# Performance work log

Measured on AMD Instinct MI355X. Metric: run time of the kernel, lower is better.

## Reference

```python
import jax, jax.numpy as jnp
import numpy as np

B, S, D, H, KD, VD, HID, L, V, OUTN = 16, 512, 512, 8, 64, 64, 2048, 4, 32000, 128
EPS = 1e-5


def _layer_norm(x, g, b):
    m = jnp.mean(x, axis=-1, keepdims=True)
    v = jnp.mean(jnp.square(x - m), axis=-1, keepdims=True)
    return (x - m) * jax.lax.rsqrt(v + EPS) * g + b


def _pos_encoding(seq_len, d_model):
    pos = jnp.arange(seq_len, dtype=jnp.float32)[:, None]
    div = jnp.exp(jnp.arange(0, d_model, 2, dtype=jnp.float32) * (-np.log(10000.0) / d_model))
    pe = jnp.zeros((seq_len, d_model), dtype=jnp.float32)
    pe = pe.at[:, 0::2].set(jnp.sin(pos * div))
    pe = pe.at[:, 1::2].set(jnp.cos(pos * div))
    return pe


def setup_inputs() -> dict:
    key = jax.random.key(0)
    ks = jax.random.split(key, 32)
    s = 0.02
    n = jax.random.normal
    inp = {
        "enc_inputs": jax.random.randint(ks[0], (B, S), 0, V, dtype=jnp.int32),
        "emb": n(ks[1], (V, D), jnp.float32) * s,
        # stacked per-layer params, leading dim = L
        "Wq": n(ks[2], (L, D, H * KD), jnp.float32) * s,
        "bq": jnp.zeros((L, H * KD), jnp.float32),
        "Wk": n(ks[3], (L, D, H * KD), jnp.float32) * s,
        "bk": jnp.zeros((L, H * KD), jnp.float32),
        "Wv": n(ks[4], (L, D, H * VD), jnp.float32) * s,
        "bv": jnp.zeros((L, H * VD), jnp.float32),
        "Wo": n(ks[5], (L, H * VD, D), jnp.float32) * s,
        "bo": jnp.zeros((L, D), jnp.float32),
        "ln1_g": jnp.ones((L, D), jnp.float32),
        "ln1_b": jnp.zeros((L, D), jnp.float32),
        "W1": n(ks[6], (L, D, HID), jnp.float32) * s,   # conv1d k=1 == linear
        "b1": jnp.zeros((L, HID), jnp.float32),
        "W2": n(ks[7], (L, HID, D), jnp.float32) * s,
        "b2": jnp.zeros((L, D), jnp.float32),
        "ln2_g": jnp.ones((L, D), jnp.float32),
        "ln2_b": jnp.zeros((L, D), jnp.float32),
        # flatten head created inside torch forward: [S*D, 128]
        "Wf": n(ks[8], (S * D, OUTN), jnp.float32) * s,
        "bf": jnp.zeros((OUTN,), jnp.float32),
        "Wout": n(ks[9], (OUTN, 1), jnp.float32) * s,
        "bout": jnp.zeros((1,), jnp.float32),
    }
    return inp


def _encoder(enc_inputs, emb, Wq, bq, Wk, bk, Wv, bv, Wo, bo, ln1_g, ln1_b,
             W1, b1, W2, b2, ln2_g, ln2_b, Wf, bf, Wout, bout):
    x = emb[enc_inputs] + _pos_encoding(S, D)[None, :, :]          # [B,S,D]
    pad = (enc_inputs == 0)[:, None, None, :]                      # [B,1,1,S]
    scale = 1.0 / np.sqrt(D)                                       # note: sqrt(embed_dim), as in source
    for l in range(L):
        # multi-head attention
        q = (x @ Wq[l] + bq[l]).reshape(B, S, H, KD)
        k = (x @ Wk[l] + bk[l]).reshape(B, S, H, KD)
        v = (x @ Wv[l] + bv[l]).reshape(B, S, H, VD)
        scores = jnp.einsum('bqhd,bkhd->bhqk', q, k) * scale
        scores = jnp.where(pad, -1e9, scores)
        attn = jax.nn.softmax(scores, axis=-1)
        ctx = jnp.einsum('bhqk,bkhd->bqhd', attn, v).reshape(B, S, H * VD)
        x = _layer_norm(ctx @ Wo[l] + bo[l] + x, ln1_g[l], ln1_b[l])
        # position-wise FFN (conv1d kernel_size=1)
        h = jax.nn.relu(x @ W1[l] + b1[l])
        x = _layer_norm(h @ W2[l] + b2[l] + x, ln2_g[l], ln2_b[l])
    flat = x.reshape(B, S * D)
    features = flat @ Wf + bf                                      # [B,128]
    y_score = jax.nn.sigmoid(features @ Wout + bout)               # [B,1]
    y_pred = jnp.round(y_score)
    return y_score, y_pred, features


def reference(enc_inputs, emb, Wq, bq, Wk, bk, Wv, bv, Wo, bo, ln1_g, ln1_b,
              W1, b1, W2, b2, ln2_g, ln2_b, Wf, bf, Wout, bout):
    return _encoder(enc_inputs, emb, Wq, bq, Wk, bk, Wv, bv, Wo, bo, ln1_g, ln1_b,
                    W1, b1, W2, b2, ln2_g, ln2_b, Wf, bf, Wout, bout)
```

## Files before the change

kernel.cpp:

```cpp
#include <hip/hip_runtime.h>
#include <hip/hip_bf16.h>
#include <math.h>

typedef unsigned short ushort_t;
typedef __attribute__((ext_vector_type(8))) short bf16x8;
typedef __attribute__((ext_vector_type(4))) float f32x4;

#define SCALE_QK 0.04419417382415922f
#define PE_C 0.017988946039015986f

__device__ __forceinline__ void g2lds16(const void* g, void* l) {
    __builtin_amdgcn_global_load_lds(
        (const __attribute__((address_space(1))) unsigned int*)g,
        (__attribute__((address_space(3))) unsigned int*)l,
        16, 0, 0);
}
__device__ __forceinline__ ushort_t f2bs(float v) {
    __hip_bfloat16 h = __float2bfloat16(v);
    return *reinterpret_cast<ushort_t*>(&h);
}
__device__ __forceinline__ float bs2f(ushort_t v) {
    return __uint_as_float(((unsigned int)v) << 16);
}

template<bool RELU, bool VT>
__global__ __launch_bounds__(512, 2) void gemm8(
    const ushort_t* __restrict__ A, const ushort_t* __restrict__ B,
    const float* __restrict__ bias, ushort_t* __restrict__ C,
    ushort_t* __restrict__ vt, int K, int lda, int ldb, int ldc)
{
    __shared__ ushort_t As[2][256 * 64];
    __shared__ ushort_t Bs[2][256 * 64];

    const int t = threadIdx.x;
    const int lane = t & 63, w = t >> 6;
    const int l16 = lane & 15, quad = lane >> 4;
    const int r8 = lane >> 3;
    const int kg = ((lane & 7) ^ r8) << 3;
    const int wm = (w >> 2) * 128;
    const int wn = (w & 3) * 64;
    const int m0 = blockIdx.y * 256, n0 = blockIdx.x * 256;
    const int NT = K >> 6;

    f32x4 acc[8][4];
    #pragma unroll
    for (int i = 0; i < 8; i++)
        #pragma unroll
        for (int j = 0; j < 4; j++)
            acc[i][j] = (f32x4){0.f, 0.f, 0.f, 0.f};

    auto STAGE8 = [&](int kt, int bb) {
        int k0 = kt << 6;
        #pragma unroll
        for (int ii = 0; ii < 4; ii++) {
            int rbase = w * 32 + ii * 8;
            g2lds16(A + (size_t)(m0 + rbase + r8) * lda + k0 + kg,
                    &As[bb][rbase * 64]);
            g2lds16(B + (size_t)(n0 + rbase + r8) * ldb + k0 + kg,
                    &Bs[bb][rbase * 64]);
        }
    };

    STAGE8(0, 0);
    STAGE8(1, 1);

    for (int kt = 0; kt < NT; kt++) {
        const int bb = kt & 1;
        if (kt < NT - 1)
            asm volatile("s_waitcnt vmcnt(8)" ::: "memory");
        else
            asm volatile("s_waitcnt vmcnt(0)" ::: "memory");
        __builtin_amdgcn_s_barrier();
        asm volatile("" ::: "memory");

        #pragma unroll
        for (int tt = 0; tt < 2; tt++) {
            bf16x8 af[8], bf[4];
            #pragma unroll
            for (int i = 0; i < 8; i++) {
                int row = wm + i * 16 + l16;
                af[i] = *(const bf16x8*)&As[bb][row * 64 + ((((tt << 2) + quad) ^ (row & 7)) << 3)];
            }
            #pragma unroll
            for (int j = 0; j < 4; j++) {
                int row = wn + j * 16 + l16;
                bf[j] = *(const bf16x8*)&Bs[bb][row * 64 + ((((tt << 2) + quad) ^ (row & 7)) << 3)];
            }
            #pragma unroll
            for (int i = 0; i < 8; i++)
                #pragma unroll
                for (int j = 0; j < 4; j++)
                    acc[i][j] = __builtin_amdgcn_mfma_f32_16x16x32_bf16(
                        af[i], bf[j], acc[i][j], 0, 0, 0);
        }

        asm volatile("" ::: "memory");
        __builtin_amdgcn_s_barrier();
        asm volatile("" ::: "memory");
        if (kt + 2 < NT)
            STAGE8(kt + 2, bb);
    }

    if (VT && n0 >= 1024) {
        #pragma unroll
        for (int i = 0; i < 8; i++) {
            int mbase = m0 + wm + i * 16 + quad * 4;
            int b = mbase >> 9, s = mbase & 511;
            #pragma unroll
            for (int j = 0; j < 4; j++) {
                int n = n0 + wn + j * 16 + l16;
                int hv = n - 1024;
                int h = hv >> 6, vd = hv & 63;
                float bv = bias[n];
                ushort4 pk;
                pk.x = f2bs(acc[i][j][0] + bv);
                pk.y = f2bs(acc[i][j][1] + bv);
                pk.z = f2bs(acc[i][j][2] + bv);
                pk.w = f2bs(acc[i][j][3] + bv);
                *(ushort4*)&vt[((size_t)((b << 3) + h)) * 32768 + (size_t)vd * 512 + s] = pk;
            }
        }
        return;
    }

    #pragma unroll
    for (int i = 0; i < 8; i++)
        #pragma unroll
        for (int j = 0; j < 4; j++) {
            int n = n0 + wn + j * 16 + l16;
            float bv = bias[n];
            #pragma unroll
            for (int r = 0; r < 4; r++) {
                int m = m0 + wm + i * 16 + quad * 4 + r;
                float v = acc[i][j][r] + bv;
                if (RELU) v = fmaxf(v, 0.f);
                C[(size_t)m * ldc + n] = f2bs(v);
            }
        }
}

__global__ __launch_bounds__(512) void gemmLN(
    const ushort_t* __restrict__ A, const ushort_t* __restrict__ B,
    const float* __restrict__ bias, const ushort_t* __restrict__ res,
    const float* __restrict__ g, const float* __restrict__ bt,
    ushort_t* __restrict__ X, int K, int lda)
{
    __shared__ ushort_t As[2][32 * 64];
    __shared__ ushort_t Bs[2][512 * 64];
    __shared__ float2 pst[8][32];
    __shared__ float2 rmv[32];

    const int t = threadIdx.x;
    const int lane = t & 63, w = t >> 6;
    const int l16 = lane & 15, quad = lane >> 4;
    const int r8 = lane >> 3;
    const int kg = ((lane & 7) ^ r8) << 3;
    const int wn = w * 64;
    const int m0 = blockIdx.x * 32;
    const int NT = K >> 6;

    f32x4 acc[2][4];
    #pragma unroll
    for (int i = 0; i < 2; i++)
        #pragma unroll
        for (int j = 0; j < 4; j++)
            acc[i][j] = (f32x4){0.f, 0.f, 0.f, 0.f};

    auto STAGE = [&](int kt, int bb) {
        int k0 = kt << 6;
        if (w < 4)
            g2lds16(A + (size_t)(m0 + w * 8 + r8) * lda + k0 + kg,
                    &As[bb][(w * 8) * 64]);
        #pragma unroll
        for (int ii = 0; ii < 8; ii++) {
            int rbase = w * 64 + ii * 8;
            g2lds16(B + (size_t)(rbase + r8) * K + k0 + kg,
                    &Bs[bb][rbase * 64]);
        }
    };

    STAGE(0, 0);
    STAGE(1, 1);

    for (int kt = 0; kt < NT; kt++) {
        const int bb = kt & 1;
        if (kt < NT - 1) {
            if (w < 4) asm volatile("s_waitcnt vmcnt(9)" ::: "memory");
            else       asm volatile("s_waitcnt vmcnt(8)" ::: "memory");
        } else {
            asm volatile("s_waitcnt vmcnt(0)" ::: "memory");
        }
        __builtin_amdgcn_s_barrier();
        asm volatile("" ::: "memory");

        #pragma unroll
        for (int tt = 0; tt < 2; tt++) {
            bf16x8 af[2], bf4[4];
            #pragma unroll
            for (int i = 0; i < 2; i++) {
                int row = i * 16 + l16;
                af[i] = *(const bf16x8*)&As[bb][row * 64 + ((((tt << 2) + quad) ^ (row & 7)) << 3)];
            }
            #pragma unroll
            for (int j = 0; j < 4; j++) {
                int row = wn + j * 16 + l16;
                bf4[j] = *(const bf16x8*)&Bs[bb][row * 64 + ((((tt << 2) + quad) ^ (row & 7)) << 3)];
            }
            #pragma unroll
            for (int i = 0; i < 2; i++)
                #pragma unroll
                for (int j = 0; j < 4; j++)
                    acc[i][j] = __builtin_amdgcn_mfma_f32_16x16x32_bf16(
                        af[i], bf4[j], acc[i][j], 0, 0, 0);
        }

        asm volatile("" ::: "memory");
        __builtin_amdgcn_s_barrier();
        asm volatile("" ::: "memory");
        if (kt + 2 < NT)
            STAGE(kt + 2, bb);
    }

    float rs[2][4], rq[2][4];
    #pragma unroll
    for (int i = 0; i < 2; i++)
        #pragma unroll
        for (int r = 0; r < 4; r++) { rs[i][r] = 0.f; rq[i][r] = 0.f; }

    #pragma unroll
    for (int i = 0; i < 2; i++)
        #pragma unroll
        for (int j = 0; j < 4; j++) {
            int n = wn + j * 16 + l16;
            float bvn = bias[n];
            #pragma unroll
            for (int r = 0; r < 4; r++) {
                int row = i * 16 + quad * 4 + r;
                float v = acc[i][j][r] + bvn
                        + bs2f(res[(size_t)(m0 + row) * 512 + n]);
                acc[i][j][r] = v;
                rs[i][r] += v;
                rq[i][r] += v * v;
            }
        }

    #pragma unroll
    for (int i = 0; i < 2; i++)
        #pragma unroll
        for (int r = 0; r < 4; r++) {
            #pragma unroll
            for (int off = 1; off < 16; off <<= 1) {
                rs[i][r] += __shfl_xor(rs[i][r], off);
                rq[i][r] += __shfl_xor(rq[i][r], off);
            }
            if (l16 == 0)
                pst[w][i * 16 + quad * 4 + r] = make_float2(rs[i][r], rq[i][r]);
        }
    __syncthreads();
    if (t < 32) {
        float s = 0.f, q = 0.f;
        #pragma unroll
        for (int wv = 0; wv < 8; wv++) {
            float2 p = pst[wv][t];
            s += p.x; q += p.y;
        }
        float mean = s * (1.f / 512.f);
        float var = q * (1.f / 512.f) - mean * mean;
        rmv[t] = make_float2(mean, rsqrtf(var + 1e-5f));
    }
    __syncthreads();

    #pragma unroll
    for (int i = 0; i < 2; i++)
        #pragma unroll
        for (int j = 0; j < 4; j++) {
            int n = wn + j * 16 + l16;
            float gn = g[n], btn = bt[n];
            #pragma unroll
            for (int r = 0; r < 4; r++) {
                int row = i * 16 + quad * 4 + r;
                float2 mr = rmv[row];
                float o = (acc[i][j][r] - mr.x) * mr.y * gn + btn;
                X[(size_t)(m0 + row) * 512 + n] = f2bs(o);
            }
        }
}

__global__ __launch_bounds__(256) void flash_attn(
    ushort_t* __restrict__ QKV, const ushort_t* __restrict__ Vt,
    const int* __restrict__ tok)
{
    __shared__ ushort_t Qs[128 * 64];
    __shared__ ushort_t Ks[128 * 64];
    __shared__ ushort_t Vts[64 * 128];
    __shared__ ushort_t Ps[128 * 128];

    const int bh = blockIdx.y;
    const int b = bh >> 3, h = bh & 7;
    const int q0 = blockIdx.x * 128;
    const int t = threadIdx.x;
    const int lane = t & 63, w = t >> 6;
    const int l16 = lane & 15, quad = lane >> 4;
    const int wm = w * 32;
    const size_t rowbase = (size_t)b * 512;

    {
        int r8 = lane >> 3;
        int kg = (lane & 7) ^ r8;
        #pragma unroll
        for (int ii = 0; ii < 4; ii++) {
            int rb = w * 32 + ii * 8;
            g2lds16(QKV + (rowbase + q0 + rb + r8) * 1536 + h * 64 + kg * 8,
                    &Qs[rb * 64]);
        }
    }

    f32x4 accO[2][4];
    #pragma unroll
    for (int i = 0; i < 2; i++)
        #pragma unroll
        for (int jv = 0; jv < 4; jv++)
            accO[i][jv] = (f32x4){0.f, 0.f, 0.f, 0.f};
    float lrow[2][4];
    #pragma unroll
    for (int i = 0; i < 2; i++)
        #pragma unroll
        for (int r = 0; r < 4; r++) lrow[i][r] = 0.f;

    for (int kc = 0; kc < 4; kc++) {
        __syncthreads();
        {
            int r8 = lane >> 3;
            int kg = (lane & 7) ^ r8;
            #pragma unroll
            for (int ii = 0; ii < 4; ii++) {
                int rb = w * 32 + ii * 8;
                g2lds16(QKV + (rowbase + kc * 128 + rb + r8) * 1536 + 512 + h * 64 + kg * 8,
                        &Ks[rb * 64]);
            }
        }
        {
            int v4 = lane >> 4;
            #pragma unroll
            for (int ii = 0; ii < 4; ii++) {
                int vb = w * 16 + ii * 4;
                int vd = vb + v4;
                int kg = (lane & 15) ^ (vd & 15);
                g2lds16(Vt + (size_t)bh * 32768 + (size_t)vd * 512 + kc * 128 + kg * 8,
                        &Vts[vb * 128]);
            }
        }
        float maskv[8];
        #pragma unroll
        for (int j = 0; j < 8; j++)
            maskv[j] = (tok[b * 512 + kc * 128 + j * 16 + l16] == 0) ? -1e9f : 0.f;

        __syncthreads();

        f32x4 sacc[2][8];
        #pragma unroll
        for (int i = 0; i < 2; i++)
            #pragma unroll
            for (int j = 0; j < 8; j++)
                sacc[i][j] = (f32x4){0.f, 0.f, 0.f, 0.f};
        #pragma unroll
        for (int tt = 0; tt < 2; tt++) {
            bf16x8 aq[2], bk8[8];
            #pragma unroll
            for (int i = 0; i < 2; i++) {
                int row = wm + i * 16 + l16;
                aq[i] = *(const bf16x8*)&Qs[row * 64 + (((tt << 2) + quad) ^ (row & 7)) * 8];
            }
            #pragma unroll
            for (int j = 0; j < 8; j++) {
                int row = j * 16 + l16;
                bk8[j] = *(const bf16x8*)&Ks[row * 64 + (((tt << 2) + quad) ^ (row & 7)) * 8];
            }
            #pragma unroll
            for (int i = 0; i < 2; i++)
                #pragma unroll
                for (int j = 0; j < 8; j++)
                    sacc[i][j] = __builtin_amdgcn_mfma_f32_16x16x32_bf16(
                        aq[i], bk8[j], sacc[i][j], 0, 0, 0);
        }

        #pragma unroll
        for (int i = 0; i < 2; i++)
            #pragma unroll
            for (int j = 0; j < 8; j++)
                #pragma unroll
                for (int r = 0; r < 4; r++) {
                    float p = __expf(fmaf(sacc[i][j][r], SCALE_QK, maskv[j]));
                    sacc[i][j][r] = p;
                    lrow[i][r] += p;
                }

        #pragma unroll
        for (int i = 0; i < 2; i++)
            #pragma unroll
            for (int j = 0; j < 8; j++) {
                int col = j * 16 + l16;
                int colc = col >> 3, csub = col & 7;
                #pragma unroll
                for (int r = 0; r < 4; r++) {
                    int row = wm + i * 16 + quad * 4 + r;
                    Ps[row * 128 + ((colc ^ (row & 15)) << 3) + csub] = f2bs(sacc[i][j][r]);
                }
            }

        #pragma unroll
        for (int tt = 0; tt < 4; tt++) {
            bf16x8 ap[2], bv8[4];
            #pragma unroll
            for (int i = 0; i < 2; i++) {
                int row = wm + i * 16 + l16;
                ap[i] = *(const bf16x8*)&Ps[row * 128 + ((((tt << 2) + quad)) ^ (row & 15)) * 8];
            }
            #pragma unroll
            for (int jv = 0; jv < 4; jv++) {
                int vd = jv * 16 + l16;
                bv8[jv] = *(const bf16x8*)&Vts[vd * 128 + (((tt << 2) + quad) ^ (vd & 15)) * 8];
            }
            #pragma unroll
            for (int i = 0; i < 2; i++)
                #pragma unroll
                for (int jv = 0; jv < 4; jv++)
                    accO[i][jv] = __builtin_amdgcn_mfma_f32_16x16x32_bf16(
                        ap[i], bv8[jv], accO[i][jv], 0, 0, 0);
        }
    }

    #pragma unroll
    for (int i = 0; i < 2; i++)
        #pragma unroll
        for (int r = 0; r < 4; r++) {
            float s = lrow[i][r];
            #pragma unroll
            for (int off = 1; off < 16; off <<= 1)
                s += __shfl_xor(s, off);
            float inv = 1.f / s;
            int row = q0 + wm + i * 16 + quad * 4 + r;
            #pragma unroll
            for (int jv = 0; jv < 4; jv++) {
                int vd = jv * 16 + l16;
                QKV[(rowbase + row) * 1536 + h * 64 + vd] = f2bs(accO[i][jv][r] * inv);
            }
        }
}

__global__ __launch_bounds__(256) void prep(
    const float* __restrict__ Wq, const float* __restrict__ Wk,
    const float* __restrict__ Wv, const float* __restrict__ Wo,
    const float* __restrict__ W1, const float* __restrict__ W2,
    const float* __restrict__ bq, const float* __restrict__ bk,
    const float* __restrict__ bv, const int* __restrict__ tok,
    const float* __restrict__ emb,
    __hip_bfloat16* __restrict__ WqkvT, __hip_bfloat16* __restrict__ WoT,
    __hip_bfloat16* __restrict__ W1T, __hip_bfloat16* __restrict__ W2T,
    float* __restrict__ bqkv, float* __restrict__ Fb,
    __hip_bfloat16* __restrict__ xb)
{
    const int blk = blockIdx.x;
    const int t = threadIdx.x;

    if (blk < 12288) {
        __shared__ float tile[32][33];
        const float* in; __hip_bfloat16* out;
        long long inz, outz; int R, Cc, bx, by, bz;
        if (blk < 4096) {
            int seg = blk >> 10, lb = blk & 1023;
            bz = lb >> 8; by = (lb >> 4) & 15; bx = lb & 15;
            R = 512; Cc = 512; inz = 262144;
            if      (seg == 0) { in = Wq; out = WqkvT;          outz = 786432; }
            else if (seg == 1) { in = Wk; out = WqkvT + 262144; outz = 786432; }
            else if (seg == 2) { in = Wv; out = WqkvT + 524288; outz = 786432; }
            else               { in = Wo; out = WoT;            outz = 262144; }
        } else if (blk < 8192) {
            int lb = blk - 4096;
            bz = lb >> 10; by = (lb >> 6) & 15; bx = lb & 63;
            R = 512; Cc = 2048; inz = 1048576; outz = 1048576;
            in = W1; out = W1T;
        } else {
            int lb = blk - 8192;
            bz = lb >> 10; by = (lb >> 4) & 63; bx = lb & 15;
            R = 2048; Cc = 512; inz = 1048576; outz = 1048576;
            in = W2; out = W2T;
        }
        in += bz * inz; out += bz * outz;
        int c0 = bx * 32, r0 = by * 32;
        int tx = t & 31, ty = t >> 5;
        #pragma unroll
        for (int i = 0; i < 4; i++)
            tile[ty + i * 8][tx] = in[(size_t)(r0 + ty + i * 8) * Cc + c0 + tx];
        __syncthreads();
        #pragma unroll
        for (int i = 0; i < 4; i++)
            out[(size_t)(c0 + ty + i * 8) * R + r0 + tx] =
                __float2bfloat16(tile[tx][ty + i * 8]);
    } else if (blk < 12312) {
        int k = blk - 12288;
        int idx = k * 256 + t;
        int l = idx / 1536, n = idx - l * 1536;
        float v = (n < 512) ? bq[l * 512 + n]
                : (n < 1024) ? bk[l * 512 + n - 512]
                             : bv[l * 512 + n - 1024];
        bqkv[idx] = v;
        if (k < 8) Fb[k * 256 + t] = 0.f;
    } else {
        int idx = (blk - 12312) * 256 + t;
        int d  = idx & 511;
        int bs = idx >> 9;
        int s  = bs & 511;
        int tk = tok[bs];
        float freq  = expf(-(float)(d & ~1) * PE_C);
        float angle = (float)s * freq;
        float pe    = (d & 1) ? cosf(angle) : sinf(angle);
        xb[idx] = __float2bfloat16(emb[(size_t)tk * 512 + d] + pe);
    }
}

__global__ __launch_bounds__(256) void feat_partial(const ushort_t* __restrict__ Xb,
                                                    const float* __restrict__ Wf,
                                                    float* __restrict__ FbP) {
    const int slice = blockIdx.x;
    const int k0 = slice * 256;
    __shared__ float Xs[16][256];
    __shared__ float RedW[4][16][128];
    const int t = threadIdx.x;

    #pragma unroll
    for (int i = 0; i < 4; i++) {
        int idx = t + i * 256;
        int b = idx >> 6, c4 = (idx & 63) * 4;
        ushort4 u = *(const ushort4*)&Xb[(size_t)b * 262144 + k0 + c4];
        Xs[b][c4 + 0] = bs2f(u.x);
        Xs[b][c4 + 1] = bs2f(u.y);
        Xs[b][c4 + 2] = bs2f(u.z);
        Xs[b][c4 + 3] = bs2f(u.w);
    }
    __syncthreads();

    const int n4 = (t & 31) * 4;
    const int kh = t >> 5;
    const int rbase = kh * 32;
    const int wv = t >> 6;
    const float* wp = Wf + (size_t)(k0 + rbase) * 128 + n4;

    float4 acc[16];
    #pragma unroll
    for (int b = 0; b < 16; b++) acc[b] = (float4){0.f, 0.f, 0.f, 0.f};

    #pragma unroll
    for (int q = 0; q < 4; q++) {
        float4 wvv[8];
        #pragma unroll
        for (int kk = 0; kk < 8; kk++)
            wvv[kk] = *(const float4*)&wp[(size_t)(q * 8 + kk) * 128];
        #pragma unroll
        for (int b = 0; b < 16; b++) {
            float4 x0 = *(const float4*)&Xs[b][rbase + q * 8];
            float4 x1 = *(const float4*)&Xs[b][rbase + q * 8 + 4];
            acc[b].x += x0.x*wvv[0].x + x0.y*wvv[1].x + x0.z*wvv[2].x + x0.w*wvv[3].x
                      + x1.x*wvv[4].x + x1.y*wvv[5].x + x1.z*wvv[6].x + x1.w*wvv[7].x;
            acc[b].y += x0.x*wvv[0].y + x0.y*wvv[1].y + x0.z*wvv[2].y + x0.w*wvv[3].y
                      + x1.x*wvv[4].y + x1.y*wvv[5].y + x1.z*wvv[6].y + x1.w*wvv[7].y;
            acc[b].z += x0.x*wvv[0].z + x0.y*wvv[1].z + x0.z*wvv[2].z + x0.w*wvv[3].z
                      + x1.x*wvv[4].z + x1.y*wvv[5].z + x1.z*wvv[6].z + x1.w*wvv[7].z;
            acc[b].w += x0.x*wvv[0].w + x0.y*wvv[1].w + x0.z*wvv[2].w + x0.w*wvv[3].w
                      + x1.x*wvv[4].w + x1.y*wvv[5].w + x1.z*wvv[6].w + x1.w*wvv[7].w;
        }
    }

    #pragma unroll
    for (int b = 0; b < 16; b++) {
        acc[b].x += __shfl_xor(acc[b].x, 32);
        acc[b].y += __shfl_xor(acc[b].y, 32);
        acc[b].z += __shfl_xor(acc[b].z, 32);
        acc[b].w += __shfl_xor(acc[b].w, 32);
    }
    if ((t & 63) < 32) {
        #pragma unroll
        for (int b = 0; b < 16; b++)
            *(float4*)&RedW[wv][b][n4] = acc[b];
    }
    __syncthreads();

    #pragma unroll
    for (int i = 0; i < 8; i++) {
        int o = t + i * 256;
        int b = o >> 7, c = o & 127;
        FbP[(size_t)slice * 2048 + o] =
            RedW[0][b][c] + RedW[1][b][c] + RedW[2][b][c] + RedW[3][b][c];
    }
}

__global__ __launch_bounds__(256) void feat_reduce(const float* __restrict__ FbP,
                                                   float* __restrict__ Fb) {
    int o = blockIdx.x * 256 + threadIdx.x;
    int g0 = blockIdx.y * 64;
    float s = 0.f;
    #pragma unroll
    for (int jj = 0; jj < 64; jj += 8) {
        float v[8];
        #pragma unroll
        for (int u = 0; u < 8; u++)
            v[u] = FbP[(size_t)(g0 + jj + u) * 2048 + o];
        #pragma unroll
        for (int u = 0; u < 8; u++) s += v[u];
    }
    atomicAdd(&Fb[o], s);
}

__global__ __launch_bounds__(256) void head_kernel(const float* __restrict__ feat,
                                                   const float* __restrict__ bfv,
                                                   const float* __restrict__ Wo2,
                                                   const float* __restrict__ bo2,
                                                   float* __restrict__ out) {
    __shared__ float f[2048];
    int t = threadIdx.x;
    for (int i = t; i < 2048; i += 256) {
        float v = feat[i] + bfv[i & 127];
        f[i] = v;
        out[32 + i] = v;
    }
    __syncthreads();
    if (t < 16) {
        float zv = bo2[0];
        for (int n = 0; n < 128; n++) zv = fmaf(f[t * 128 + n], Wo2[n], zv);
        float ys = 1.f / (1.f + expf(-zv));
        out[t] = ys;
        out[16 + t] = rintf(ys);
    }
}

extern "C" void kernel_launch(void* const* d_in, const int* in_sizes, int n_in,
                              void* d_out, int out_size, void* d_ws, size_t ws_size,
                              hipStream_t stream) {
    const int*   enc  = (const int*)  d_in[0];
    const float* emb  = (const float*)d_in[1];
    const float* Wq   = (const float*)d_in[2];
    const float* bq   = (const float*)d_in[3];
    const float* Wk   = (const float*)d_in[4];
    const float* bk   = (const float*)d_in[5];
    const float* Wv   = (const float*)d_in[6];
    const float* bv   = (const float*)d_in[7];
    const float* Wo   = (const float*)d_in[8];
    const float* bo   = (const float*)d_in[9];
    const float* g1   = (const float*)d_in[10];
    const float* be1  = (const float*)d_in[11];
    const float* W1   = (const float*)d_in[12];
    const float* b1f  = (const float*)d_in[13];
    const float* W2   = (const float*)d_in[14];
    const float* b2f  = (const float*)d_in[15];
    const float* g2   = (const float*)d_in[16];
    const float* be2  = (const float*)d_in[17];
    const float* Wf   = (const float*)d_in[18];
    const float* bf   = (const float*)d_in[19];
    const float* Wout = (const float*)d_in[20];
    const float* bout = (const float*)d_in[21];
    float* out = (float*)d_out;

    char* ws = (char*)d_ws;
    ushort_t* Xb   = (ushort_t*) (ws + 16777216);
    ushort_t* QKV  = (ushort_t*) (ws + 25165824);
    ushort_t* Vt   = (ushort_t*) (ws + 50331648);
    ushort_t* S    = (ushort_t*) (ws + 58720256);
    ushort_t* WqkvT= (ushort_t*) (ws + 92274688);
    ushort_t* WoT  = (ushort_t*) (ws + 98566144);
    ushort_t* W1T  = (ushort_t*) (ws + 100663296);
    ushort_t* W2T  = (ushort_t*) (ws + 109051904);
    float*    bqkv = (float*)    (ws + 117440512);
    float*    Fb   = (float*)    (ws + 117465088);
    float*    FbP  = (float*)    (ws + 0);

    typedef __hip_bfloat16 bf16;

    prep<<<28696, 256, 0, stream>>>(
        Wq, Wk, Wv, Wo, W1, W2, bq, bk, bv, enc, emb,
        (bf16*)WqkvT, (bf16*)WoT, (bf16*)W1T, (bf16*)W2T, bqkv, Fb, (bf16*)Xb);

    for (int l = 0; l < 4; l++) {
        gemm8<false, true><<<dim3(6, 32), 512, 0, stream>>>(
            Xb, WqkvT + (size_t)l * 786432, bqkv + l * 1536,
            QKV, Vt, 512, 512, 512, 1536);

        flash_attn<<<dim3(4, 128), 256, 0, stream>>>(QKV, Vt, enc);

        gemmLN<<<256, 512, 0, stream>>>(
            QKV, WoT + (size_t)l * 262144, bo + l * 512, Xb,
            g1 + l * 512, be1 + l * 512, Xb, 512, 1536);

        gemm8<true, false><<<dim3(8, 32), 512, 0, stream>>>(
            Xb, W1T + (size_t)l * 1048576, b1f + l * 2048,
            S, nullptr, 512, 512, 512, 2048);

        gemmLN<<<256, 512, 0, stream>>>(
            S, W2T + (size_t)l * 1048576, b2f + l * 512, Xb,
            g2 + l * 512, be2 + l * 512, Xb, 2048, 2048);
    }

    feat_partial<<<1024, 256, 0, stream>>>(Xb, Wf, FbP);
    feat_reduce<<<dim3(8, 16), 256, 0, stream>>>(FbP, Fb);
    head_kernel<<<1, 256, 0, stream>>>(Fb, bf, Wout, bout, out);
}
```

Baseline: 902.5 us.

## Split fused GEMM+LayerNorm into 128x128-tiled GEMM plus separate LN kernel

Replaces the full-row 32x512 GEMM+LayerNorm kernel with a 128x128-tiled GEMM that writes the pre-norm bf16 output and per-row partial sum/sumsq. A new lightweight kernel then combines the partials and applies LayerNorm. The aim is better operand reuse, 256 blocks at 2 blocks per CU, and less LDS per block. The cost is an extra kernel launch and an extra round trip of the activation through memory. Flash attention now aliases K into the P buffer to cut LDS usage, with an added barrier before P is written.

```diff
diff --git a/kernel.cpp b/kernel.cpp
--- a/kernel.cpp
+++ b/kernel.cpp
@@ -139,42 +139,40 @@
         }
 }
 
-__global__ __launch_bounds__(512) void gemmLN(
+__global__ __launch_bounds__(256, 2) void gemm4(
     const ushort_t* __restrict__ A, const ushort_t* __restrict__ B,
-    const float* __restrict__ bias, const ushort_t* __restrict__ res,
-    const float* __restrict__ g, const float* __restrict__ bt,
-    ushort_t* __restrict__ X, int K, int lda)
+    const float* __restrict__ bias, const ushort_t* __restrict__ resb,
+    ushort_t* __restrict__ C, float2* __restrict__ part,
+    int K, int lda, int ldb, int ldc)
 {
-    __shared__ ushort_t As[2][32 * 64];
-    __shared__ ushort_t Bs[2][512 * 64];
-    __shared__ float2 pst[8][32];
-    __shared__ float2 rmv[32];
+    __shared__ ushort_t As[2][128 * 64];
+    __shared__ ushort_t Bs[2][128 * 64];
 
     const int t = threadIdx.x;
     const int lane = t & 63, w = t >> 6;
     const int l16 = lane & 15, quad = lane >> 4;
     const int r8 = lane >> 3;
     const int kg = ((lane & 7) ^ r8) << 3;
-    const int wn = w * 64;
-    const int m0 = blockIdx.x * 32;
+    const int wm = (w >> 1) * 64;
+    const int wn = (w & 1) * 64;
+    const int m0 = blockIdx.y * 128, n0 = blockIdx.x * 128;
     const int NT = K >> 6;
 
-    f32x4 acc[2][4];
-    #pragma unroll
-    for (int i = 0; i < 2; i++)
+    f32x4 acc[4][4];
+    #pragma unroll
+    for (int i = 0; i < 4; i++)
         #pragma unroll
         for (int j = 0; j < 4; j++)
             acc[i][j] = (f32x4){0.f, 0.f, 0.f, 0.f};
 
     auto STAGE = [&](int kt, int bb) {
         int k0 = kt << 6;
-        if (w < 4)
-            g2lds16(A + (size_t)(m0 + w * 8 + r8) * lda + k0 + kg,
-                    &As[bb][(w * 8) * 64]);
-        #pragma unroll
-        for (int ii = 0; ii < 8; ii++) {
-            int rbase = w * 64 + ii * 8;
-            g2lds16(B + (size_t)(rbase + r8) * K + k0 + kg,
+        #pragma unroll
+        for (int ii = 0; ii < 4; ii++) {
+            int rbase = w * 32 + ii * 8;
+            g2lds16(A + (size_t)(m0 + rbase + r8) * lda + k0 + kg,
+                    &As[bb][rbase * 64]);
+            g2lds16(B + (size_t)(n0 + rbase + r8) * ldb + k0 + kg,
                     &Bs[bb][rbase * 64]);
         }
     };
@@ -184,34 +182,32 @@
 
     for (int kt = 0; kt < NT; kt++) {
         const int bb = kt & 1;
-        if (kt < NT - 1) {
-            if (w < 4) asm volatile("s_waitcnt vmcnt(9)" ::: "memory");
-            else       asm volatile("s_waitcnt vmcnt(8)" ::: "memory");
-        } else {
+        if (kt < NT - 1)
+            asm volatile("s_waitcnt vmcnt(8)" ::: "memory");
+        else
             asm volatile("s_waitcnt vmcnt(0)" ::: "memory");
-        }
         __builtin_amdgcn_s_barrier();
         asm volatile("" ::: "memory");
 
         #pragma unroll
         for (int tt = 0; tt < 2; tt++) {
-            bf16x8 af[2], bf4[4];
-            #pragma unroll
-            for (int i = 0; i < 2; i++) {
-                int row = i * 16 + l16;
+            bf16x8 af[4], bf[4];
+            #pragma unroll
+            for (int i = 0; i < 4; i++) {
+                int row = wm + i * 16 + l16;
                 af[i] = *(const bf16x8*)&As[bb][row * 64 + ((((tt << 2) + quad) ^ (row & 7)) << 3)];
             }
             #pragma unroll
             for (int j = 0; j < 4; j++) {
                 int row = wn + j * 16 + l16;
-                bf4[j] = *(const bf16x8*)&Bs[bb][row * 64 + ((((tt << 2) + quad) ^ (row & 7)) << 3)];
-            }
-            #pragma unroll
-            for (int i = 0; i < 2; i++)
+                bf[j] = *(const bf16x8*)&Bs[bb][row * 64 + ((((tt << 2) + quad) ^ (row & 7)) << 3)];
+            }
+            #pragma unroll
+            for (int i = 0; i < 4; i++)
                 #pragma unroll
                 for (int j = 0; j < 4; j++)
                     acc[i][j] = __builtin_amdgcn_mfma_f32_16x16x32_bf16(
-                        af[i], bf4[j], acc[i][j], 0, 0, 0);
+                        af[i], bf[j], acc[i][j], 0, 0, 0);
         }
 
         asm volatile("" ::: "memory");
@@ -221,69 +217,69 @@
             STAGE(kt + 2, bb);
     }
 
-    float rs[2][4], rq[2][4];
-    #pragma unroll
-    for (int i = 0; i < 2; i++)
-        #pragma unroll
-        for (int r = 0; r < 4; r++) { rs[i][r] = 0.f; rq[i][r] = 0.f; }
-
-    #pragma unroll
-    for (int i = 0; i < 2; i++)
+    #pragma unroll
+    for (int i = 0; i < 4; i++) {
+        float rs[4] = {0.f, 0.f, 0.f, 0.f}, rq[4] = {0.f, 0.f, 0.f, 0.f};
         #pragma unroll
         for (int j = 0; j < 4; j++) {
-            int n = wn + j * 16 + l16;
-            float bvn = bias[n];
+            int n = n0 + wn + j * 16 + l16;
+            float bv = bias[n];
             #pragma unroll
             for (int r = 0; r < 4; r++) {
-                int row = i * 16 + quad * 4 + r;
-                float v = acc[i][j][r] + bvn
-                        + bs2f(res[(size_t)(m0 + row) * 512 + n]);
-                acc[i][j][r] = v;
-                rs[i][r] += v;
-                rq[i][r] += v * v;
-            }
-        }
-
-    #pragma unroll
-    for (int i = 0; i < 2; i++)
+                int m = m0 + wm + i * 16 + quad * 4 + r;
+                float v = acc[i][j][r] + bv + bs2f(resb[(size_t)m * ldc + n]);
+                C[(size_t)m * ldc + n] = f2bs(v);
+                rs[r] += v; rq[r] += v * v;
+            }
+        }
         #pragma unroll
         for (int r = 0; r < 4; r++) {
+            float s = rs[r], q = rq[r];
             #pragma unroll
             for (int off = 1; off < 16; off <<= 1) {
-                rs[i][r] += __shfl_xor(rs[i][r], off);
-                rq[i][r] += __shfl_xor(rq[i][r], off);
-            }
-            if (l16 == 0)
-                pst[w][i * 16 + quad * 4 + r] = make_float2(rs[i][r], rq[i][r]);
-        }
-    __syncthreads();
-    if (t < 32) {
-        float s = 0.f, q = 0.f;
-        #pragma unroll
-        for (int wv = 0; wv < 8; wv++) {
-            float2 p = pst[wv][t];
-            s += p.x; q += p.y;
-        }
+                s += __shfl_xor(s, off);
+                q += __shfl_xor(q, off);
+            }
+            if (l16 == 0) {
+                int m = m0 + wm + i * 16 + quad * 4 + r;
+                part[(size_t)m * 8 + blockIdx.x * 2 + (w & 1)] = make_float2(s, q);
+            }
+        }
+    }
+}
+
+__global__ __launch_bounds__(256) void ln_stats(const ushort_t* __restrict__ Cpre,
+                                                const float2* __restrict__ part,
+                                                const float* __restrict__ g,
+                                                const float* __restrict__ b,
+                                                ushort_t* __restrict__ Xb) {
+    long long row = blockIdx.x;
+    int t = threadIdx.x;
+    float s = 0.f, q = 0.f;
+    if (t < 8) {
+        float2 p = part[row * 8 + t];
+        s = p.x; q = p.y;
+    }
+    #pragma unroll
+    for (int off = 1; off < 8; off <<= 1) {
+        s += __shfl_xor(s, off);
+        q += __shfl_xor(q, off);
+    }
+    __shared__ float mv[2];
+    if (t == 0) {
         float mean = s * (1.f / 512.f);
         float var = q * (1.f / 512.f) - mean * mean;
-        rmv[t] = make_float2(mean, rsqrtf(var + 1e-5f));
+        mv[0] = mean;
+        mv[1] = rsqrtf(var + 1e-5f);
     }
     __syncthreads();
-
-    #pragma unroll
-    for (int i = 0; i < 2; i++)
-        #pragma unroll
-        for (int j = 0; j < 4; j++) {
-            int n = wn + j * 16 + l16;
-            float gn = g[n], btn = bt[n];
-            #pragma unroll
-            for (int r = 0; r < 4; r++) {
-                int row = i * 16 + quad * 4 + r;
-                float2 mr = rmv[row];
-                float o = (acc[i][j][r] - mr.x) * mr.y * gn + btn;
-                X[(size_t)(m0 + row) * 512 + n] = f2bs(o);
-            }
-        }
+    float mean = mv[0], r = mv[1];
+    int c = t * 2;
+    ushort2 u = *(const ushort2*)&Cpre[row * 512 + c];
+    ushort2 o;
+    o.x = f2bs((bs2f(u.x) - mean) * r * g[c]     + b[c]);
+    o.y = f2bs((bs2f(u.y) - mean) * r * g[c + 1] + b[c + 1]);
+    *(ushort2*)&Xb[row * 512 + c] = o;
 }
 
 __global__ __launch_bounds__(256) void flash_attn(
@@ -291,9 +287,9 @@
     const int* __restrict__ tok)
 {
     __shared__ ushort_t Qs[128 * 64];
-    __shared__ ushort_t Ks[128 * 64];
+    __shared__ ushort_t Ps[128 * 128];
     __shared__ ushort_t Vts[64 * 128];
-    __shared__ ushort_t Ps[128 * 128];
+    ushort_t* Ks = Ps;
 
     const int bh = blockIdx.y;
     const int b = bh >> 3, h = bh & 7;
@@ -394,6 +390,8 @@
                     sacc[i][j][r] = p;
                     lrow[i][r] += p;
                 }
+
+        __syncthreads();
 
         #pragma unroll
         for (int i = 0; i < 2; i++)
@@ -661,6 +659,8 @@
     float* out = (float*)d_out;
 
     char* ws = (char*)d_ws;
+    ushort_t* Cpre = (ushort_t*) (ws + 0);
+    float*    FbP  = (float*)    (ws + 0);
     ushort_t* Xb   = (ushort_t*) (ws + 16777216);
     ushort_t* QKV  = (ushort_t*) (ws + 25165824);
     ushort_t* Vt   = (ushort_t*) (ws + 50331648);
@@ -671,7 +671,7 @@
     ushort_t* W2T  = (ushort_t*) (ws + 109051904);
     float*    bqkv = (float*)    (ws + 117440512);
     float*    Fb   = (float*)    (ws + 117465088);
-    float*    FbP  = (float*)    (ws + 0);
+    float2*   part = (float2*)   (ws + 117473280);
 
     typedef __hip_bfloat16 bf16;
 
@@ -686,17 +686,19 @@
 
         flash_attn<<<dim3(4, 128), 256, 0, stream>>>(QKV, Vt, enc);
 
-        gemmLN<<<256, 512, 0, stream>>>(
+        gemm4<<<dim3(4, 64), 256, 0, stream>>>(
             QKV, WoT + (size_t)l * 262144, bo + l * 512, Xb,
-            g1 + l * 512, be1 + l * 512, Xb, 512, 1536);
+            Cpre, part, 512, 1536, 512, 512);
+        ln_stats<<<8192, 256, 0, stream>>>(Cpre, part, g1 + l * 512, be1 + l * 512, Xb);
 
         gemm8<true, false><<<dim3(8, 32), 512, 0, stream>>>(
             Xb, W1T + (size_t)l * 1048576, b1f + l * 2048,
             S, nullptr, 512, 512, 512, 2048);
 
-        gemmLN<<<256, 512, 0, stream>>>(
+        gemm4<<<dim3(4, 64), 256, 0, stream>>>(
             S, W2T + (size_t)l * 1048576, b2f + l * 512, Xb,
-            g2 + l * 512, be2 + l * 512, Xb, 2048, 2048);
+            Cpre, part, 2048, 2048, 2048, 512);
+        ln_stats<<<8192, 256, 0, stream>>>(Cpre, part, g2 + l * 512, be2 + l * 512, Xb);
     }
 
     feat_partial<<<1024, 256, 0, stream>>>(Xb, Wf, FbP);
```

New measurement: 961.0 us. 6.5% more time.
